# Kernel optimization log

Hardware: AMD Instinct MI355X
Metric: run time of the kernel (lower is better)

## Reference

```python
import jax, jax.numpy as jnp
import numpy as np
import math

FEAT_DIM, M, K = 512, 64, 256
D = FEAT_DIM // M  # 8
ALPHA = 1.0
B = 16384


def setup_inputs() -> dict:
    key = jax.random.key(0)
    kx, kc = jax.random.split(key)
    x = jax.random.normal(kx, (B, FEAT_DIM), dtype=jnp.float32)
    # Codebook: unit-norm codewords scaled by 1/sqrt(M), mimicking the
    # normalized-hypersphere init (orthogonal rotation / permutation do not
    # change the math, only the values).
    c = jax.random.normal(kc, (M, K, D), dtype=jnp.float32)
    c = c / jnp.linalg.norm(c, axis=-1, keepdims=True) / math.sqrt(M)
    return {"x": x, "C": c}


def reference(x, C):
    # x: (B, feat_dim) -> (B, M, D)
    x_ = x.reshape(x.shape[0], M, D)
    # per-subspace inner products with codewords: (B, M, K)
    ips = jnp.einsum('bmd,mkd->bmk', x_, C)
    # training-mode straight-through assignment
    soft = jax.nn.softmax(ips * (M / ALPHA), axis=-1)
    hard = jax.nn.one_hot(jnp.argmax(ips, axis=-1), K, dtype=ips.dtype)
    codes = jax.lax.stop_gradient(hard - soft) + soft
    # reconstruction: (B, M, D) -> (B, feat_dim)
    x_hat = jnp.einsum('mkd,bmk->bmd', C, codes).reshape(x.shape[0], -1)
    return x_hat, codes
```

## Files before the change

kernel.cpp:

```cpp
#include <hip/hip_runtime.h>
#include <math.h>


#define B_SZ   16384
#define FEAT   512
#define M_SZ   64
#define K_SZ   256
#define D_SZ   8

typedef float v4f __attribute__((ext_vector_type(4)));

__global__ __launch_bounds__(256) void pq_fused(
    const float* __restrict__ x,
    const float* __restrict__ C,
    float* __restrict__ xhat,
    float* __restrict__ codes)
{
#pragma clang fp contract(off)

    const int t     = threadIdx.x;
    const int m     = blockIdx.x & (M_SZ - 1);
    const int chunk = blockIdx.x >> 6;
    const int base  = (chunk << 10) | t;

    __shared__ v4f Cs[K_SZ * 2];
    __shared__ unsigned char lbk[1024];

    {
        const v4f* src = (const v4f*)(C + (size_t)m * (K_SZ * D_SZ)) + (t << 1);
        Cs[(t << 1) | 0] = src[0];
        Cs[(t << 1) | 1] = src[1];
    }

    const float* xp0 = x + (size_t)base * FEAT + m * D_SZ;
    const float* xp1 = xp0 + (size_t)256 * FEAT;
    const float* xp2 = xp1 + (size_t)256 * FEAT;
    const float* xp3 = xp2 + (size_t)256 * FEAT;
    const v4f xa0 = ((const v4f*)xp0)[0], xb0 = ((const v4f*)xp0)[1];
    const v4f xa1 = ((const v4f*)xp1)[0], xb1 = ((const v4f*)xp1)[1];
    const v4f xa2 = ((const v4f*)xp2)[0], xb2 = ((const v4f*)xp2)[1];
    const v4f xa3 = ((const v4f*)xp3)[0], xb3 = ((const v4f*)xp3)[1];

    __syncthreads();

    float best0 = -INFINITY, best1 = -INFINITY;
    float best2 = -INFINITY, best3 = -INFINITY;
    int   bk0 = 0, bk1 = 0, bk2 = 0, bk3 = 0;

#pragma unroll 2
    for (int k = 0; k < K_SZ; ++k) {
        const v4f ca = Cs[(k << 1) | 0];
        const v4f cb = Cs[(k << 1) | 1];

        v4f P0 = xa0 * ca, Q0 = xb0 * cb, T0 = P0 + Q0;
        float d0 = (T0.x + T0.y) + (T0.z + T0.w);
        v4f P1 = xa1 * ca, Q1 = xb1 * cb, T1 = P1 + Q1;
        float d1 = (T1.x + T1.y) + (T1.z + T1.w);
        v4f P2 = xa2 * ca, Q2 = xb2 * cb, T2 = P2 + Q2;
        float d2 = (T2.x + T2.y) + (T2.z + T2.w);
        v4f P3 = xa3 * ca, Q3 = xb3 * cb, T3 = P3 + Q3;
        float d3 = (T3.x + T3.y) + (T3.z + T3.w);

        if (d0 > best0) { best0 = d0; bk0 = k; }
        if (d1 > best1) { best1 = d1; bk1 = k; }
        if (d2 > best2) { best2 = d2; bk2 = k; }
        if (d3 > best3) { best3 = d3; bk3 = k; }
    }

    {
        float* xh0 = xhat + (size_t)base * FEAT + m * D_SZ;
        ((v4f*)xh0)[0] = Cs[(bk0 << 1) | 0];
        ((v4f*)xh0)[1] = Cs[(bk0 << 1) | 1];
        float* xh1 = xh0 + (size_t)256 * FEAT;
        ((v4f*)xh1)[0] = Cs[(bk1 << 1) | 0];
        ((v4f*)xh1)[1] = Cs[(bk1 << 1) | 1];
        float* xh2 = xh1 + (size_t)256 * FEAT;
        ((v4f*)xh2)[0] = Cs[(bk2 << 1) | 0];
        ((v4f*)xh2)[1] = Cs[(bk2 << 1) | 1];
        float* xh3 = xh2 + (size_t)256 * FEAT;
        ((v4f*)xh3)[0] = Cs[(bk3 << 1) | 0];
        ((v4f*)xh3)[1] = Cs[(bk3 << 1) | 1];
    }

    lbk[t]       = (unsigned char)bk0;
    lbk[t + 256] = (unsigned char)bk1;
    lbk[t + 512] = (unsigned char)bk2;
    lbk[t + 768] = (unsigned char)bk3;
    __syncthreads();

    const int w     = t >> 6;
    const int lane  = t & 63;
    const int lane4 = lane << 2;

#pragma unroll 4
    for (int j = 0; j < 256; ++j) {
        const int i  = (j << 2) | w;
        const int kk = (int)lbk[i];
        float4 v;
        v.x = (kk == lane4 + 0) ? 1.0f : 0.0f;
        v.y = (kk == lane4 + 1) ? 1.0f : 0.0f;
        v.z = (kk == lane4 + 2) ? 1.0f : 0.0f;
        v.w = (kk == lane4 + 3) ? 1.0f : 0.0f;
        const size_t f4 = ((size_t)((chunk << 10) | i) << 12) + (m << 6) + lane;
        ((float4*)codes)[f4] = v;
    }
}

extern "C" void kernel_launch(void* const* d_in, const int* in_sizes, int n_in,
                              void* d_out, int out_size, void* d_ws, size_t ws_size,
                              hipStream_t stream)
{
    const float* x = (const float*)d_in[0];
    const float* C = (const float*)d_in[1];
    float* xhat  = (float*)d_out;
    float* codes = (float*)d_out + (size_t)B_SZ * FEAT;

    hipLaunchKernelGGL(pq_fused, dim3(1024), dim3(256), 0, stream,
                       x, C, xhat, codes);
}
```

Measured before the change: 1.152 ms.

## Regroup blocks over 8 subspaces and 256 rows for contiguous writes

Each block now covers 8 subspaces and 256 rows, with 512 threads (one wave per subspace). Each block holds 8 codebooks in shared memory, and the launch is 512 blocks instead of 1024. Codes rows are written as contiguous 8 KB stretches using nontemporal stores. The xhat writes are restaged so each row's 64-float segment is written coalesced. This targets memory write efficiency on the large codes output. In exchange, shared memory per block rises to 64 KB, which may limit occupancy.

```diff
diff --git a/kernel.cpp b/kernel.cpp
--- a/kernel.cpp
+++ b/kernel.cpp
@@ -10,7 +10,7 @@
 
 typedef float v4f __attribute__((ext_vector_type(4)));
 
-__global__ __launch_bounds__(256) void pq_fused(
+__global__ __launch_bounds__(512) void pq_fused(
     const float* __restrict__ x,
     const float* __restrict__ C,
     float* __restrict__ xhat,
@@ -18,24 +18,27 @@
 {
 #pragma clang fp contract(off)
 
-    const int t     = threadIdx.x;
-    const int m     = blockIdx.x & (M_SZ - 1);
-    const int chunk = blockIdx.x >> 6;
-    const int base  = (chunk << 10) | t;
+    const int t  = threadIdx.x;
+    const int w  = t >> 6;
+    const int l  = t & 63;
+    const int mg = blockIdx.x & 7;
+    const int rc = blockIdx.x >> 3;
 
-    __shared__ v4f Cs[K_SZ * 2];
-    __shared__ unsigned char lbk[1024];
+    __shared__ v4f           Cs[8 * K_SZ * 2];
+    __shared__ unsigned char lbk[256 * 8];
 
     {
-        const v4f* src = (const v4f*)(C + (size_t)m * (K_SZ * D_SZ)) + (t << 1);
-        Cs[(t << 1) | 0] = src[0];
-        Cs[(t << 1) | 1] = src[1];
+        const v4f* src = (const v4f*)(C + (size_t)mg * (8 * K_SZ * D_SZ));
+#pragma unroll
+        for (int j = 0; j < 8; ++j)
+            Cs[(j << 9) + t] = src[(j << 9) + t];
     }
 
-    const float* xp0 = x + (size_t)base * FEAT + m * D_SZ;
-    const float* xp1 = xp0 + (size_t)256 * FEAT;
-    const float* xp2 = xp1 + (size_t)256 * FEAT;
-    const float* xp3 = xp2 + (size_t)256 * FEAT;
+    const int m = (mg << 3) | w;
+    const float* xp0 = x + ((size_t)((rc << 8) | l)) * FEAT + m * D_SZ;
+    const float* xp1 = xp0 + (size_t)64 * FEAT;
+    const float* xp2 = xp1 + (size_t)64 * FEAT;
+    const float* xp3 = xp2 + (size_t)64 * FEAT;
     const v4f xa0 = ((const v4f*)xp0)[0], xb0 = ((const v4f*)xp0)[1];
     const v4f xa1 = ((const v4f*)xp1)[0], xb1 = ((const v4f*)xp1)[1];
     const v4f xa2 = ((const v4f*)xp2)[0], xb2 = ((const v4f*)xp2)[1];
@@ -43,14 +46,15 @@
 
     __syncthreads();
 
+    const v4f* Cw = &Cs[w << 9];
     float best0 = -INFINITY, best1 = -INFINITY;
     float best2 = -INFINITY, best3 = -INFINITY;
     int   bk0 = 0, bk1 = 0, bk2 = 0, bk3 = 0;
 
 #pragma unroll 2
     for (int k = 0; k < K_SZ; ++k) {
-        const v4f ca = Cs[(k << 1) | 0];
-        const v4f cb = Cs[(k << 1) | 1];
+        const v4f ca = Cw[(k << 1) | 0];
+        const v4f cb = Cw[(k << 1) | 1];
 
         v4f P0 = xa0 * ca, Q0 = xb0 * cb, T0 = P0 + Q0;
         float d0 = (T0.x + T0.y) + (T0.z + T0.w);
@@ -67,42 +71,40 @@
         if (d3 > best3) { best3 = d3; bk3 = k; }
     }
 
-    {
-        float* xh0 = xhat + (size_t)base * FEAT + m * D_SZ;
-        ((v4f*)xh0)[0] = Cs[(bk0 << 1) | 0];
-        ((v4f*)xh0)[1] = Cs[(bk0 << 1) | 1];
-        float* xh1 = xh0 + (size_t)256 * FEAT;
-        ((v4f*)xh1)[0] = Cs[(bk1 << 1) | 0];
-        ((v4f*)xh1)[1] = Cs[(bk1 << 1) | 1];
-        float* xh2 = xh1 + (size_t)256 * FEAT;
-        ((v4f*)xh2)[0] = Cs[(bk2 << 1) | 0];
-        ((v4f*)xh2)[1] = Cs[(bk2 << 1) | 1];
-        float* xh3 = xh2 + (size_t)256 * FEAT;
-        ((v4f*)xh3)[0] = Cs[(bk3 << 1) | 0];
-        ((v4f*)xh3)[1] = Cs[(bk3 << 1) | 1];
-    }
-
-    lbk[t]       = (unsigned char)bk0;
-    lbk[t + 256] = (unsigned char)bk1;
-    lbk[t + 512] = (unsigned char)bk2;
-    lbk[t + 768] = (unsigned char)bk3;
+    lbk[((l      ) << 3) | w] = (unsigned char)bk0;
+    lbk[((l +  64) << 3) | w] = (unsigned char)bk1;
+    lbk[((l + 128) << 3) | w] = (unsigned char)bk2;
+    lbk[((l + 192) << 3) | w] = (unsigned char)bk3;
     __syncthreads();
 
-    const int w     = t >> 6;
-    const int lane  = t & 63;
-    const int lane4 = lane << 2;
+    const int lane4 = l << 2;
+    v4f* const cbase = (v4f*)codes + ((size_t)rc << 20) + (size_t)((mg << 9) + t);
 
 #pragma unroll 4
-    for (int j = 0; j < 256; ++j) {
-        const int i  = (j << 2) | w;
-        const int kk = (int)lbk[i];
-        float4 v;
+    for (int r = 0; r < 256; ++r) {
+        const int kk = (int)lbk[(r << 3) | w];
+        v4f v;
         v.x = (kk == lane4 + 0) ? 1.0f : 0.0f;
         v.y = (kk == lane4 + 1) ? 1.0f : 0.0f;
         v.z = (kk == lane4 + 2) ? 1.0f : 0.0f;
         v.w = (kk == lane4 + 3) ? 1.0f : 0.0f;
-        const size_t f4 = ((size_t)((chunk << 10) | i) << 12) + (m << 6) + lane;
-        ((float4*)codes)[f4] = v;
+        __builtin_nontemporal_store(v, cbase + ((size_t)r << 12));
+    }
+
+    {
+        const int j    = t & 15;
+        const int m_l  = j >> 1;
+        const int h    = j & 1;
+        const int rb   = t >> 4;
+        const v4f* Cm_ = &Cs[m_l << 9];
+#pragma unroll
+        for (int c = 0; c < 8; ++c) {
+            const int r  = rb + (c << 5);
+            const int kk = (int)lbk[(r << 3) | m_l];
+            v4f* dst = (v4f*)(xhat + ((size_t)((rc << 8) | r)) * FEAT
+                              + (mg << 6) + (j << 2));
+            *dst = Cm_[(kk << 1) | h];
+        }
     }
 }
 
@@ -115,6 +117,6 @@
     float* xhat  = (float*)d_out;
     float* codes = (float*)d_out + (size_t)B_SZ * FEAT;
 
-    hipLaunchKernelGGL(pq_fused, dim3(1024), dim3(256), 0, stream,
+    hipLaunchKernelGGL(pq_fused, dim3(512), dim3(512), 0, stream,
                        x, C, xhat, codes);
 }
```

After: 1.160 ms. No clear change (+0.7%).
